# Optimization experiments

Measured on AMD Instinct MI355X. Metric: run time of the kernel, lower is better.

Reference implementation:

```python
import jax, jax.numpy as jnp
import numpy as np

N, E, C = 50000, 300000, 256  # nodes, edges, hidden size


def setup_inputs() -> dict:
    key = jax.random.key(0)
    ks = jax.random.split(key, 12)
    s = 0.05  # param init scale
    return {
        "x": jax.random.normal(ks[0], (N, C), dtype=jnp.float32),
        "edge_index": jax.random.randint(ks[1], (2, E), 0, N, dtype=jnp.int32),
        # GATConv layer 1 (heads=1): shared lin weight, att_src/att_dst vectors, bias
        "W1": jax.random.normal(ks[2], (C, C), dtype=jnp.float32) * s,
        "a1_src": jax.random.normal(ks[3], (C,), dtype=jnp.float32) * s,
        "a1_dst": jax.random.normal(ks[4], (C,), dtype=jnp.float32) * s,
        "b1": jnp.zeros((C,), dtype=jnp.float32),
        # GATConv layer 2
        "W2": jax.random.normal(ks[5], (C, C), dtype=jnp.float32) * s,
        "a2_src": jax.random.normal(ks[6], (C,), dtype=jnp.float32) * s,
        "a2_dst": jax.random.normal(ks[7], (C,), dtype=jnp.float32) * s,
        "b2": jnp.zeros((C,), dtype=jnp.float32),
        # Final Linear (torch convention: W [out, in], y = x @ W.T + b)
        "Wl": jax.random.normal(ks[8], (C, C), dtype=jnp.float32) * s,
        "bl": jnp.zeros((C,), dtype=jnp.float32),
    }


def _gat_conv(x, src, dst, W, a_src, a_dst, b):
    # PyG GATConv, heads=1, negative_slope=0.2, self-loops already appended.
    h = x @ W                                  # [N, C]
    alpha_src = h @ a_src                      # [N]
    alpha_dst = h @ a_dst                      # [N]
    e = jax.nn.leaky_relu(alpha_src[src] + alpha_dst[dst], 0.2)   # [E']
    # numerically stable softmax over incoming edges of each destination node
    m = jax.ops.segment_max(e, dst, num_segments=N)               # [N]
    ex = jnp.exp(e - m[dst])
    den = jax.ops.segment_sum(ex, dst, num_segments=N)            # [N]
    w = ex / den[dst]                                              # [E']
    out = jax.ops.segment_sum(h[src] * w[:, None], dst, num_segments=N)  # [N, C]
    return out + b


def reference(x, edge_index, W1, a1_src, a1_dst, b1, W2, a2_src, a2_dst, b2, Wl, bl):
    # add_self_loops (done inside each GATConv in PyG; appending once to the
    # input edge list is equivalent since both convs see the same edges)
    loops = jnp.arange(N, dtype=edge_index.dtype)
    ei = jnp.concatenate([edge_index, jnp.stack([loops, loops])], axis=1)
    src, dst = ei[0], ei[1]
    x = jax.nn.relu(_gat_conv(x, src, dst, W1, a1_src, a1_dst, b1))
    x = jax.nn.relu(_gat_conv(x, src, dst, W2, a2_src, a2_dst, b2))
    return x @ Wl.T + bl
```

## Files before the change

kernel.cpp:

```cpp
#include <hip/hip_runtime.h>

#define NN 50000
#define EE 300000
#define ET (EE + NN)
#define CD 256
#define PAD_M 50176
#define BCAP 64

typedef unsigned short ushortT;
typedef short bf16x8 __attribute__((ext_vector_type(8)));
typedef float f32x4 __attribute__((ext_vector_type(4)));

__device__ __forceinline__ ushortT f2b(float f) {
    unsigned u = __builtin_bit_cast(unsigned, f);
    unsigned r = (u + 0x7FFFu + ((u >> 16) & 1u)) >> 16;
    return (ushortT)r;
}
__device__ __forceinline__ float b2f(ushortT b) {
    return __builtin_bit_cast(float, ((unsigned)b) << 16);
}


__global__ __launch_bounds__(256) void wvec_kernel(
    const float* __restrict__ W1, const float* __restrict__ a1s,
    const float* __restrict__ a1d, const float* __restrict__ W2,
    const float* __restrict__ a2s, const float* __restrict__ a2d,
    float* __restrict__ w1s, float* __restrict__ w1d,
    float* __restrict__ w2s, float* __restrict__ w2d,
    int* __restrict__ cnt) {
    int b = blockIdx.x;
    int g = b * 256 + threadIdx.x;
    if (g < NN) cnt[g] = 0;
    if (g + 32768 < NN) cnt[g + 32768] = 0;

    const float* W = (b < 64) ? W1 : W2;
    const float* vs = (b < 64) ? a1s : a2s;
    const float* vd = (b < 64) ? a1d : a2d;
    float* os = (b < 64) ? w1s : w2s;
    float* od = (b < 64) ? w1d : w2d;
    int r = (b & 63) * 4 + (threadIdx.x >> 6);
    int lane = threadIdx.x & 63;
    float4 wv = *(const float4*)(W + (size_t)r * CD + lane * 4);
    float4 s4 = *(const float4*)(vs + lane * 4);
    float4 d4 = *(const float4*)(vd + lane * 4);
    float ss = wv.x * s4.x + wv.y * s4.y + wv.z * s4.z + wv.w * s4.w;
    float dd = wv.x * d4.x + wv.y * d4.y + wv.z * d4.z + wv.w * d4.w;
#pragma unroll
    for (int off = 1; off < 64; off <<= 1) {
        ss += __shfl_xor(ss, off);
        dd += __shfl_xor(dd, off);
    }
    if (lane == 0) {
        os[r] = ss;
        od[r] = dd;
    }
}

#define PREP_X 12500
#define PREP_W1 12564
#define PREP_W2 12628
#define PREP_END 12692

__global__ __launch_bounds__(256) void prep_kernel(
    const float* __restrict__ x, const float* __restrict__ W1,
    const float* __restrict__ W2, const float* __restrict__ Wl,
    ushortT* __restrict__ B0, ushortT* __restrict__ W1t,
    ushortT* __restrict__ W2t, ushortT* __restrict__ Wlt,
    const float* __restrict__ w1s, const float* __restrict__ w1d,
    float* __restrict__ as1, float* __restrict__ ad1) {
    __shared__ float t[32][33];
    int b = blockIdx.x, tidx = threadIdx.x;
    if (b < PREP_X) {
        int node = b * 4 + (tidx >> 6);
        int lane = tidx & 63;
        float4 v = *(const float4*)(x + (size_t)node * CD + lane * 4);
        ushort4 o;
        o.x = f2b(v.x); o.y = f2b(v.y); o.z = f2b(v.z); o.w = f2b(v.w);
        *(ushort4*)(B0 + (size_t)node * CD + lane * 4) = o;
        float4 s4 = *(const float4*)(w1s + lane * 4);
        float4 d4 = *(const float4*)(w1d + lane * 4);
        float ss = v.x * s4.x + v.y * s4.y + v.z * s4.z + v.w * s4.w;
        float dd = v.x * d4.x + v.y * d4.y + v.z * d4.z + v.w * d4.w;
#pragma unroll
        for (int off = 1; off < 64; off <<= 1) {
            ss += __shfl_xor(ss, off);
            dd += __shfl_xor(dd, off);
        }
        if (lane == 0) {
            as1[node] = ss;
            ad1[node] = dd;
        }
    } else if (b < PREP_W2) {
        const float* W = (b < PREP_W1) ? W1 : W2;
        ushortT* Bt = (b < PREP_W1) ? W1t : W2t;
        int rel = b - ((b < PREP_W1) ? PREP_X : PREP_W1);
        int bx = (rel & 7) * 32;
        int by = (rel >> 3) * 32;
        int xx = tidx & 31, yy = tidx >> 5;
        for (int y = yy; y < 32; y += 8) t[y][xx] = W[(size_t)(bx + y) * CD + by + xx];
        __syncthreads();
        for (int y = yy; y < 32; y += 8)
            Bt[(size_t)(by + y) * CD + bx + xx] = f2b(t[xx][y]);
    } else {
        int id = (b - PREP_W2) * 256 + tidx;
        float4 v = *(const float4*)(Wl + (size_t)id * 4);
        ushort4 o;
        o.x = f2b(v.x); o.y = f2b(v.y); o.z = f2b(v.z); o.w = f2b(v.w);
        *(ushort4*)(Wlt + (size_t)id * 4) = o;
    }
}


__global__ void fill_bucket(const int* __restrict__ ei, int* __restrict__ cnt,
                            int* __restrict__ srcs) {
    int i = blockIdx.x * blockDim.x + threadIdx.x;
    if (i < EE) {
        int s = ei[i];
        int d = ei[EE + i];
        int p = atomicAdd(&cnt[d], 1);
        if (p < BCAP) srcs[((size_t)d << 6) + p] = s;
    } else if (i < ET) {
        int n = i - EE;
        int p = atomicAdd(&cnt[n], 1);
        if (p < BCAP) srcs[((size_t)n << 6) + p] = n;
    }
}


template <int OUTF32>
__global__ __launch_bounds__(256, 4) void gemm_mfma(const ushortT* __restrict__ A,
                                                    const ushortT* __restrict__ Bt,
                                                    const float* __restrict__ bias,
                                                    float* __restrict__ outF,
                                                    ushortT* __restrict__ outB,
                                                    int M) {
    __shared__ ushortT Bs[64 * 256];
    int tid = threadIdx.x;
    int wave = tid >> 6, lane = tid & 63;
    int wm = wave * 32;
    int bid = blockIdx.x;
    int id = (bid & 7) * 196 + (bid >> 3);
    int bm = (id >> 2) * 128, bn = (id & 3) * 64;
    int l15 = lane & 15, quad = lane >> 4;

#pragma unroll
    for (int p = 0; p < 8; ++p) {
        int c = p * 256 + tid;
        int slot = c >> 5;
        int piece = c & 31;
        int col = (slot & 15) * 4 + (slot >> 4);
        int spiece = piece ^ (slot & 31);
        const ushortT* gb = Bt + (size_t)(bn + col) * CD + spiece * 8;
        __builtin_amdgcn_global_load_lds(
            (const __attribute__((address_space(1))) void*)gb,
            (__attribute__((address_space(3))) void*)(Bs + (size_t)(p * 256 + wave * 64) * 8),
            16, 0, 0);
    }

    bf16x8 a[2][8];
#pragma unroll
    for (int kk = 0; kk < 8; ++kk)
#pragma unroll
        for (int i = 0; i < 2; ++i)
            a[i][kk] = *(const bf16x8*)(A + (size_t)(bm + wm + i * 16 + l15) * CD + kk * 32 + quad * 8);

    __syncthreads();

    f32x4 acc[2][4] = {};

#pragma unroll
    for (int kk = 0; kk < 8; ++kk) {
        bf16x8 b[4];
        int kc = kk * 4 + quad;
#pragma unroll
        for (int j = 0; j < 4; ++j) {
            int slot = j * 16 + l15;
            b[j] = *(const bf16x8*)(Bs + (size_t)slot * 256 + (size_t)(kc ^ (slot & 31)) * 8);
        }
#pragma unroll
        for (int i = 0; i < 2; ++i)
#pragma unroll
            for (int j = 0; j < 4; ++j)
                acc[i][j] = __builtin_amdgcn_mfma_f32_16x16x32_bf16(a[i][kk], b[j], acc[i][j], 0, 0, 0);
    }

    int colb = bn + l15 * 4;
#pragma unroll
    for (int i = 0; i < 2; ++i) {
#pragma unroll
        for (int r = 0; r < 4; ++r) {
            int row = bm + wm + i * 16 + quad * 4 + r;
            if (OUTF32) {
                if (row < M) {
                    float4 bv = *(const float4*)(bias + colb);
                    float4 v;
                    v.x = acc[i][0][r] + bv.x;
                    v.y = acc[i][1][r] + bv.y;
                    v.z = acc[i][2][r] + bv.z;
                    v.w = acc[i][3][r] + bv.w;
                    *(float4*)(outF + (size_t)row * CD + colb) = v;
                }
            } else {
                ushort4 o;
                o.x = f2b(acc[i][0][r]);
                o.y = f2b(acc[i][1][r]);
                o.z = f2b(acc[i][2][r]);
                o.w = f2b(acc[i][3][r]);
                *(ushort4*)(outB + (size_t)row * CD + colb) = o;
            }
        }
    }
}


__device__ __forceinline__ float lrelu02(float x) { return x > 0.f ? x : 0.2f * x; }

template <int ALPHA2>
__global__ __launch_bounds__(256) void gat_agg(const ushortT* __restrict__ h,
                                               const float* __restrict__ as_,
                                               const float* __restrict__ ad_,
                                               const int* __restrict__ cnt,
                                               const int* __restrict__ srcs,
                                               const float* __restrict__ bias,
                                               ushortT* __restrict__ out,
                                               const float* __restrict__ w2s,
                                               const float* __restrict__ w2d,
                                               float* __restrict__ as_n,
                                               float* __restrict__ ad_n) {
    int node = blockIdx.x * 8 + (threadIdx.x >> 5);
    int hl = threadIdx.x & 31;
    if (node >= NN) return;
    int deg = cnt[node];
    if (deg > BCAP) deg = BCAP;
    int rs = node << 6;
    float adst = ad_[node];

    float acc[8] = {0.f, 0.f, 0.f, 0.f, 0.f, 0.f, 0.f, 0.f};

    int maxdeg = max(deg, __shfl_xor(deg, 32));

    if (maxdeg <= 32) {
        int s_lane = srcs[rs + ((hl < deg) ? hl : 0)];

        int s0[8];
#pragma unroll
        for (int t = 0; t < 8; ++t) s0[t] = __shfl(s_lane, (t < deg) ? t : 0, 32);
        bf16x8 hv[8];
#pragma unroll
        for (int t = 0; t < 8; ++t)
            hv[t] = *(const bf16x8*)(h + (size_t)s0[t] * CD + hl * 8);

        float e = (hl < deg) ? lrelu02(as_[s_lane] + adst) : -1e30f;
        float m = e;
#pragma unroll
        for (int off = 1; off < 32; off <<= 1) m = fmaxf(m, __shfl_xor(m, off));
        float ex = (hl < deg) ? __expf(e - m) : 0.f;
        float den = ex;
#pragma unroll
        for (int off = 1; off < 32; off <<= 1) den += __shfl_xor(den, off);
        float wl = ex / den;

#pragma unroll
        for (int t = 0; t < 8; ++t) {
            float wv = __shfl(wl, t, 32);
            wv = (t < deg) ? wv : 0.f;
#pragma unroll
            for (int c = 0; c < 8; ++c)
                acc[c] += wv * b2f((ushortT)hv[t][c]);
        }

        for (int kk = 8; kk < maxdeg; kk += 8) {
            int s[8];
            float w[8];
#pragma unroll
            for (int t = 0; t < 8; ++t) {
                int idx = kk + t;
                int ii = (idx < deg) ? idx : 0;
                int sv = __shfl(s_lane, ii, 32);
                float wv = __shfl(wl, ii, 32);
                s[t] = sv;
                w[t] = (idx < deg) ? wv : 0.f;
            }
            bf16x8 hv2[8];
#pragma unroll
            for (int t = 0; t < 8; ++t)
                hv2[t] = *(const bf16x8*)(h + (size_t)s[t] * CD + hl * 8);
#pragma unroll
            for (int t = 0; t < 8; ++t) {
#pragma unroll
                for (int c = 0; c < 8; ++c)
                    acc[c] += w[t] * b2f((ushortT)hv2[t][c]);
            }
        }
    } else {
        int re = rs + deg;
        float m = -1e30f;
        for (int k = rs + hl; k < re; k += 32) {
            float e = lrelu02(as_[srcs[k]] + adst);
            m = fmaxf(m, e);
        }
#pragma unroll
        for (int off = 1; off < 32; off <<= 1) m = fmaxf(m, __shfl_xor(m, off));
        float den = 0.f;
        for (int k = rs + hl; k < re; k += 32) {
            float e = lrelu02(as_[srcs[k]] + adst);
            den += __expf(e - m);
        }
#pragma unroll
        for (int off = 1; off < 32; off <<= 1) den += __shfl_xor(den, off);
        float inv_den = 1.f / den;
        for (int k = rs; k < re; ++k) {
            int sv = srcs[k];
            float e = lrelu02(as_[sv] + adst);
            float wv = __expf(e - m) * inv_den;
            bf16x8 hv = *(const bf16x8*)(h + (size_t)sv * CD + hl * 8);
#pragma unroll
            for (int c = 0; c < 8; ++c)
                acc[c] += wv * b2f((ushortT)hv[c]);
        }
    }

    float4 bv0 = *(const float4*)(bias + hl * 8);
    float4 bv1 = *(const float4*)(bias + hl * 8 + 4);
    float r[8];
    r[0] = fmaxf(acc[0] + bv0.x, 0.f);
    r[1] = fmaxf(acc[1] + bv0.y, 0.f);
    r[2] = fmaxf(acc[2] + bv0.z, 0.f);
    r[3] = fmaxf(acc[3] + bv0.w, 0.f);
    r[4] = fmaxf(acc[4] + bv1.x, 0.f);
    r[5] = fmaxf(acc[5] + bv1.y, 0.f);
    r[6] = fmaxf(acc[6] + bv1.z, 0.f);
    r[7] = fmaxf(acc[7] + bv1.w, 0.f);
    bf16x8 o;
#pragma unroll
    for (int c = 0; c < 8; ++c) o[c] = (short)f2b(r[c]);
    *(bf16x8*)(out + (size_t)node * CD + hl * 8) = o;

    if (ALPHA2) {
        float4 s0 = *(const float4*)(w2s + hl * 8);
        float4 s1 = *(const float4*)(w2s + hl * 8 + 4);
        float4 d0 = *(const float4*)(w2d + hl * 8);
        float4 d1 = *(const float4*)(w2d + hl * 8 + 4);
        float ss = r[0] * s0.x + r[1] * s0.y + r[2] * s0.z + r[3] * s0.w +
                   r[4] * s1.x + r[5] * s1.y + r[6] * s1.z + r[7] * s1.w;
        float dd = r[0] * d0.x + r[1] * d0.y + r[2] * d0.z + r[3] * d0.w +
                   r[4] * d1.x + r[5] * d1.y + r[6] * d1.z + r[7] * d1.w;
#pragma unroll
        for (int off = 1; off < 32; off <<= 1) {
            ss += __shfl_xor(ss, off);
            dd += __shfl_xor(dd, off);
        }
        if (hl == 0) {
            as_n[node] = ss;
            ad_n[node] = dd;
        }
    }
}


extern "C" void kernel_launch(void* const* d_in, const int* in_sizes, int n_in,
                              void* d_out, int out_size, void* d_ws, size_t ws_size,
                              hipStream_t stream) {
    const float* x = (const float*)d_in[0];
    const int* ei = (const int*)d_in[1];
    const float* W1 = (const float*)d_in[2];
    const float* a1s = (const float*)d_in[3];
    const float* a1d = (const float*)d_in[4];
    const float* b1 = (const float*)d_in[5];
    const float* W2 = (const float*)d_in[6];
    const float* a2s = (const float*)d_in[7];
    const float* a2d = (const float*)d_in[8];
    const float* b2 = (const float*)d_in[9];
    const float* Wl = (const float*)d_in[10];
    const float* bl = (const float*)d_in[11];
    float* out = (float*)d_out;

    char* w = (char*)d_ws;
    ushortT* B0 = (ushortT*)w; w += (size_t)PAD_M * CD * 2;
    ushortT* B1 = (ushortT*)w; w += (size_t)PAD_M * CD * 2;
    ushortT* B2 = (ushortT*)w; w += (size_t)PAD_M * CD * 2;
    ushortT* W1t = (ushortT*)w; w += (size_t)CD * CD * 2;
    ushortT* W2t = (ushortT*)w; w += (size_t)CD * CD * 2;
    ushortT* Wlt = (ushortT*)w; w += (size_t)CD * CD * 2;
    float* as1 = (float*)w; w += (size_t)NN * 4;
    float* ad1 = (float*)w; w += (size_t)NN * 4;
    float* as2 = (float*)w; w += (size_t)NN * 4;
    float* ad2 = (float*)w; w += (size_t)NN * 4;
    float* w1s = (float*)w; w += CD * 4;
    float* w1d = (float*)w; w += CD * 4;
    float* w2s = (float*)w; w += CD * 4;
    float* w2d = (float*)w; w += CD * 4;
    int* cnt = (int*)w; w += (size_t)NN * 4;
    int* srcs = (int*)w; w += (size_t)NN * BCAP * 4;

    wvec_kernel<<<128, 256, 0, stream>>>(W1, a1s, a1d, W2, a2s, a2d,
                                         w1s, w1d, w2s, w2d, cnt);

    prep_kernel<<<PREP_END, 256, 0, stream>>>(x, W1, W2, Wl, B0, W1t, W2t, Wlt,
                                              w1s, w1d, as1, ad1);

    fill_bucket<<<(ET + 255) / 256, 256, 0, stream>>>(ei, cnt, srcs);

    int ggrid = (PAD_M / 128) * 4;
    int nagg_blocks = (NN + 7) / 8;

    gemm_mfma<0><<<ggrid, 256, 0, stream>>>(B0, W1t, nullptr, nullptr, B1, NN);
    gat_agg<1><<<nagg_blocks, 256, 0, stream>>>(B1, as1, ad1, cnt, srcs,
                                                b1, B2, w2s, w2d, as2, ad2);

    gemm_mfma<0><<<ggrid, 256, 0, stream>>>(B2, W2t, nullptr, nullptr, B1, NN);
    gat_agg<0><<<nagg_blocks, 256, 0, stream>>>(B1, as2, ad2, cnt, srcs,
                                                b2, B0, nullptr, nullptr,
                                                nullptr, nullptr);

    gemm_mfma<1><<<ggrid, 256, 0, stream>>>(B0, Wlt, bl, out, nullptr, NN);
}
```

Measured before the change: 259.8 us.

## Pre-swizzle weights into chunked layout, drop LDS staging, fuse bucket fill into prep

Result: slower. 295.3 us (+13.7%).

```diff
diff --git a/kernel.cpp b/kernel.cpp
--- a/kernel.cpp
+++ b/kernel.cpp
@@ -59,7 +59,8 @@
 #define PREP_X 12500
 #define PREP_W1 12564
 #define PREP_W2 12628
-#define PREP_END 12692
+#define PREP_WL 12660
+#define PREP_END 14028
 
 __global__ __launch_bounds__(256) void prep_kernel(
     const float* __restrict__ x, const float* __restrict__ W1,
@@ -67,7 +68,9 @@
     ushortT* __restrict__ B0, ushortT* __restrict__ W1t,
     ushortT* __restrict__ W2t, ushortT* __restrict__ Wlt,
     const float* __restrict__ w1s, const float* __restrict__ w1d,
-    float* __restrict__ as1, float* __restrict__ ad1) {
+    float* __restrict__ as1, float* __restrict__ ad1,
+    const int* __restrict__ ei, int* __restrict__ cnt,
+    int* __restrict__ srcs) {
     __shared__ float t[32][33];
     int b = blockIdx.x, tidx = threadIdx.x;
     if (b < PREP_X) {
@@ -99,42 +102,51 @@
         int xx = tidx & 31, yy = tidx >> 5;
         for (int y = yy; y < 32; y += 8) t[y][xx] = W[(size_t)(bx + y) * CD + by + xx];
         __syncthreads();
-        for (int y = yy; y < 32; y += 8)
-            Bt[(size_t)(by + y) * CD + bx + xx] = f2b(t[xx][y]);
+        if (tidx < 128) {
+            int nl = tidx & 31;
+            int kg = tidx >> 5;
+            int chunk = (bx >> 3) + kg;
+            ushortT o[8];
+#pragma unroll
+            for (int e = 0; e < 8; ++e) o[e] = f2b(t[kg * 8 + e][nl]);
+            *(ushort4*)(Bt + (size_t)chunk * 2048 + (size_t)(by + nl) * 8) =
+                *(const ushort4*)&o[0];
+            *(ushort4*)(Bt + (size_t)chunk * 2048 + (size_t)(by + nl) * 8 + 4) =
+                *(const ushort4*)&o[4];
+        }
+    } else if (b < PREP_WL) {
+        int chunk = b - PREP_W2;
+        int n = tidx;
+        float4 f0 = *(const float4*)(Wl + (size_t)n * CD + chunk * 8);
+        float4 f1 = *(const float4*)(Wl + (size_t)n * CD + chunk * 8 + 4);
+        ushortT o[8];
+        o[0] = f2b(f0.x); o[1] = f2b(f0.y); o[2] = f2b(f0.z); o[3] = f2b(f0.w);
+        o[4] = f2b(f1.x); o[5] = f2b(f1.y); o[6] = f2b(f1.z); o[7] = f2b(f1.w);
+        *(ushort4*)(Wlt + (size_t)chunk * 2048 + (size_t)n * 8) = *(const ushort4*)&o[0];
+        *(ushort4*)(Wlt + (size_t)chunk * 2048 + (size_t)n * 8 + 4) = *(const ushort4*)&o[4];
     } else {
-        int id = (b - PREP_W2) * 256 + tidx;
-        float4 v = *(const float4*)(Wl + (size_t)id * 4);
-        ushort4 o;
-        o.x = f2b(v.x); o.y = f2b(v.y); o.z = f2b(v.z); o.w = f2b(v.w);
-        *(ushort4*)(Wlt + (size_t)id * 4) = o;
-    }
-}
-
-
-__global__ void fill_bucket(const int* __restrict__ ei, int* __restrict__ cnt,
-                            int* __restrict__ srcs) {
-    int i = blockIdx.x * blockDim.x + threadIdx.x;
-    if (i < EE) {
-        int s = ei[i];
-        int d = ei[EE + i];
-        int p = atomicAdd(&cnt[d], 1);
-        if (p < BCAP) srcs[((size_t)d << 6) + p] = s;
-    } else if (i < ET) {
-        int n = i - EE;
-        int p = atomicAdd(&cnt[n], 1);
-        if (p < BCAP) srcs[((size_t)n << 6) + p] = n;
+        int i = (b - PREP_WL) * 256 + tidx;
+        if (i < EE) {
+            int s = ei[i];
+            int d = ei[EE + i];
+            int p = atomicAdd(&cnt[d], 1);
+            if (p < BCAP) srcs[((size_t)d << 6) + p] = s;
+        } else if (i < ET) {
+            int n = i - EE;
+            int p = atomicAdd(&cnt[n], 1);
+            if (p < BCAP) srcs[((size_t)n << 6) + p] = n;
+        }
     }
 }
 
 
 template <int OUTF32>
-__global__ __launch_bounds__(256, 4) void gemm_mfma(const ushortT* __restrict__ A,
-                                                    const ushortT* __restrict__ Bt,
+__global__ __launch_bounds__(256, 3) void gemm_mfma(const ushortT* __restrict__ A,
+                                                    const ushortT* __restrict__ Bf,
                                                     const float* __restrict__ bias,
                                                     float* __restrict__ outF,
                                                     ushortT* __restrict__ outB,
                                                     int M) {
-    __shared__ ushortT Bs[64 * 256];
     int tid = threadIdx.x;
     int wave = tid >> 6, lane = tid & 63;
     int wm = wave * 32;
@@ -143,20 +155,6 @@
     int bm = (id >> 2) * 128, bn = (id & 3) * 64;
     int l15 = lane & 15, quad = lane >> 4;
 
-#pragma unroll
-    for (int p = 0; p < 8; ++p) {
-        int c = p * 256 + tid;
-        int slot = c >> 5;
-        int piece = c & 31;
-        int col = (slot & 15) * 4 + (slot >> 4);
-        int spiece = piece ^ (slot & 31);
-        const ushortT* gb = Bt + (size_t)(bn + col) * CD + spiece * 8;
-        __builtin_amdgcn_global_load_lds(
-            (const __attribute__((address_space(1))) void*)gb,
-            (__attribute__((address_space(3))) void*)(Bs + (size_t)(p * 256 + wave * 64) * 8),
-            16, 0, 0);
-    }
-
     bf16x8 a[2][8];
 #pragma unroll
     for (int kk = 0; kk < 8; ++kk)
@@ -164,19 +162,15 @@
         for (int i = 0; i < 2; ++i)
             a[i][kk] = *(const bf16x8*)(A + (size_t)(bm + wm + i * 16 + l15) * CD + kk * 32 + quad * 8);
 
-    __syncthreads();
-
     f32x4 acc[2][4] = {};
 
 #pragma unroll
     for (int kk = 0; kk < 8; ++kk) {
+        int chunk = kk * 4 + quad;
         bf16x8 b[4];
-        int kc = kk * 4 + quad;
-#pragma unroll
-        for (int j = 0; j < 4; ++j) {
-            int slot = j * 16 + l15;
-            b[j] = *(const bf16x8*)(Bs + (size_t)slot * 256 + (size_t)(kc ^ (slot & 31)) * 8);
-        }
+#pragma unroll
+        for (int j = 0; j < 4; ++j)
+            b[j] = *(const bf16x8*)(Bf + (size_t)chunk * 2048 + (size_t)(bn + l15 * 4 + j) * 8);
 #pragma unroll
         for (int i = 0; i < 2; ++i)
 #pragma unroll
@@ -397,9 +391,7 @@
                                          w1s, w1d, w2s, w2d, cnt);
 
     prep_kernel<<<PREP_END, 256, 0, stream>>>(x, W1, W2, Wl, B0, W1t, W2t, Wlt,
-                                              w1s, w1d, as1, ad1);
-
-    fill_bucket<<<(ET + 255) / 256, 256, 0, stream>>>(ei, cnt, srcs);
+                                              w1s, w1d, as1, ad1, ei, cnt, srcs);
 
     int ggrid = (PAD_M / 128) * 4;
     int nagg_blocks = (NN + 7) / 8;
```
